# Kernel optimization log

Hardware: AMD Instinct MI355X
Metric: run time of the kernel (lower is better)

Reference implementation:

```python
import jax, jax.numpy as jnp
import numpy as np
import math

NUM_HEADS = 8
SR_RATIO = 2
LN_EPS = 1e-5


def setup_inputs() -> dict:
    key = jax.random.key(0)
    ks = jax.random.split(key, 8)
    B, H, W, C = 2, 64, 64, 512
    N = H * W
    M = (H // SR_RATIO) * (W // SR_RATIO)  # 1024, K/V feature dim after SR reshape
    units = C  # num_heads * head_dim
    s = 0.02
    return {
        "x": jax.random.normal(ks[0], (B, N, C), jnp.float32),
        "Wq": jax.random.normal(ks[1], (C, units), jnp.float32) * s,
        "bq": jnp.zeros((units,), jnp.float32),
        "Wconv": jax.random.normal(ks[2], (C, C, SR_RATIO, SR_RATIO), jnp.float32) * s,  # OIHW
        "bconv": jnp.zeros((C,), jnp.float32),
        "gamma": jnp.ones((M,), jnp.float32),
        "beta": jnp.zeros((M,), jnp.float32),
        "Wkv": jax.random.normal(ks[3], (M, 2 * units), jnp.float32) * s,
        "bkv": jnp.zeros((2 * units,), jnp.float32),
        "Wproj": jax.random.normal(ks[4], (units, C), jnp.float32) * s,
        "bproj": jnp.zeros((C,), jnp.float32),
        "H": H,
        "W": W,
    }


def reference(x, Wq, bq, Wconv, bconv, gamma, beta, Wkv, bkv, Wproj, bproj, H, W):
    B, N, C = x.shape
    nh = NUM_HEADS
    hd = C // nh
    units = nh * hd
    sr = SR_RATIO

    # Q: [B, nh, N, hd]
    q = (x @ Wq + bq).reshape(B, N, nh, hd).transpose(0, 2, 1, 3)

    # Spatial reduction on K/V: x -> [B, C, H, W] -> conv(stride=sr) -> [B, C, H/sr, W/sr]
    xi = x.transpose(0, 2, 1).reshape(B, C, H, W)
    xc = jax.lax.conv_general_dilated(
        xi, Wconv, window_strides=(sr, sr), padding="VALID",
        dimension_numbers=("NCHW", "OIHW", "NCHW"))
    xc = xc + bconv[None, :, None, None]
    x_ = xc.reshape(B, C, -1)  # [B, C, M]; K/V seq len = C, feature dim = M
    mu = jnp.mean(x_, axis=-1, keepdims=True)
    var = jnp.mean(jnp.square(x_ - mu), axis=-1, keepdims=True)
    x_ = (x_ - mu) * jax.lax.rsqrt(var + LN_EPS) * gamma + beta

    # KV: [B, C, 2*units] -> [2, B, nh, C, hd]
    kv = (x_ @ Wkv + bkv).reshape(B, C, 2, nh, hd).transpose(2, 0, 3, 1, 4)
    k, v = kv[0], kv[1]  # each [B, nh, C, hd]

    attn = jnp.einsum("bhnd,bhmd->bhnm", q, k) / jnp.asarray(math.sqrt(hd), x.dtype)
    attn = jax.nn.softmax(attn, axis=-1)  # [B, nh, N, C]

    out = jnp.einsum("bhnm,bhmd->bhnd", attn, v)  # [B, nh, N, hd]
    # Faithful to original: transpose to [B, nh, hd, N] then row-major reshape to [B, N, units]
    out = out.transpose(0, 1, 3, 2).reshape(B, -1, units)
    out = out @ Wproj + bproj  # [B, N, C]
    return out
```

## Files before the change

### kernel.cpp

```cpp
#include <hip/hip_runtime.h>


#define B_    2
#define NTOK  4096
#define C_    512
#define MSP   1024
#define NH    8
#define HD    64

typedef __attribute__((ext_vector_type(8))) short short8;
typedef __attribute__((ext_vector_type(4))) short short4v;
typedef __attribute__((ext_vector_type(4))) float f32x4;

__device__ __forceinline__ unsigned short f2bf(float f) {
    unsigned u = __builtin_bit_cast(unsigned, f);
    u += 0x7FFFu + ((u >> 16) & 1u);
    return (unsigned short)(u >> 16);
}

__global__ __launch_bounds__(256) void convert_bf16(
    const float* __restrict__ in, unsigned short* __restrict__ out, int n8)
{
    int i = blockIdx.x * 256 + threadIdx.x;
    if (i >= n8) return;
    float4 a = ((const float4*)in)[2 * i];
    float4 b = ((const float4*)in)[2 * i + 1];
    short8 o;
    o[0] = (short)f2bf(a.x); o[1] = (short)f2bf(a.y);
    o[2] = (short)f2bf(a.z); o[3] = (short)f2bf(a.w);
    o[4] = (short)f2bf(b.x); o[5] = (short)f2bf(b.y);
    o[6] = (short)f2bf(b.z); o[7] = (short)f2bf(b.w);
    ((short8*)out)[i] = o;
}

__global__ __launch_bounds__(256) void transpose_convert(
    const float* __restrict__ in, unsigned short* __restrict__ out, int R, int C)
{
    __shared__ float T[64][68];
    const int tid = threadIdx.x;
    const int r0 = blockIdx.y * 64, c0 = blockIdx.x * 64;
    const int i = tid >> 2, jp = tid & 3;
    #pragma unroll
    for (int q = 0; q < 4; ++q) {
        float4 v = *(const float4*)(in + (long)(r0 + i) * C + c0 + jp * 16 + q * 4);
        *(float4*)&T[i][jp * 16 + q * 4] = v;
    }
    __syncthreads();
    #pragma unroll
    for (int q = 0; q < 4; ++q) {
        short4v o;
        #pragma unroll
        for (int l = 0; l < 4; ++l)
            o[l] = (short)f2bf(T[jp * 16 + q * 4 + l][i]);
        *(short4v*)(out + (long)(c0 + i) * R + r0 + jp * 16 + q * 4) = o;
    }
}

__global__ __launch_bounds__(256) void gather_kernel(
    const float* __restrict__ x, unsigned short* __restrict__ xg)
{
    const int tid = threadIdx.x;
    const int ty = tid >> 4, tx = tid & 15;
    const int m = blockIdx.x * 16 + ty;
    const int b = blockIdx.y;
    const int my = m >> 5, mx = m & 31;
    const float* xb_ = x + (long)b * NTOK * C_;
    unsigned short* op = xg + ((long)b * MSP + m) * 2048;
    const float* p00 = xb_ + (long)((2 * my + 0) * 64 + 2 * mx + 0) * C_;
    const float* p01 = xb_ + (long)((2 * my + 0) * 64 + 2 * mx + 1) * C_;
    const float* p10 = xb_ + (long)((2 * my + 1) * 64 + 2 * mx + 0) * C_;
    const float* p11 = xb_ + (long)((2 * my + 1) * 64 + 2 * mx + 1) * C_;
    for (int c0 = tx * 4; c0 < C_; c0 += 64) {
        float4 v0 = *(const float4*)(p00 + c0);
        float4 v1 = *(const float4*)(p01 + c0);
        float4 v2 = *(const float4*)(p10 + c0);
        float4 v3 = *(const float4*)(p11 + c0);
        short8 o0, o1;
        o0[0] = (short)f2bf(v0.x); o0[1] = (short)f2bf(v1.x);
        o0[2] = (short)f2bf(v2.x); o0[3] = (short)f2bf(v3.x);
        o0[4] = (short)f2bf(v0.y); o0[5] = (short)f2bf(v1.y);
        o0[6] = (short)f2bf(v2.y); o0[7] = (short)f2bf(v3.y);
        o1[0] = (short)f2bf(v0.z); o1[1] = (short)f2bf(v1.z);
        o1[2] = (short)f2bf(v2.z); o1[3] = (short)f2bf(v3.z);
        o1[4] = (short)f2bf(v0.w); o1[5] = (short)f2bf(v1.w);
        o1[6] = (short)f2bf(v2.w); o1[7] = (short)f2bf(v3.w);
        *(short8*)(op + 4 * c0) = o0;
        *(short8*)(op + 4 * c0 + 8) = o1;
    }
}

template<int OMODE>
__global__ __launch_bounds__(256) void gemm_bf16(
    const unsigned short* __restrict__ A, const unsigned short* __restrict__ BT,
    const float* __restrict__ bias, void* __restrict__ Cv,
    int M, int N, int Kc, int KS, int lda, int ldb, int ldc,
    long sAb, long sBb, long sCb)
{
    __shared__ unsigned short As[128][72];
    __shared__ unsigned short Bs[128][72];
    const int tid = threadIdx.x;
    const int z = blockIdx.z, b = z / KS, kc = z % KS;
    const int row0 = blockIdx.y * 128, col0 = blockIdx.x * 128;
    const unsigned short* Ap = A + b * sAb + (long)kc * Kc + (long)row0 * lda;
    const unsigned short* Bp = BT + b * sBb + (long)kc * Kc + (long)col0 * ldb;
    const int lane = tid & 63, wave = tid >> 6;
    const int wr = (wave >> 1) * 64, wc = (wave & 1) * 64;
    const int l15 = lane & 15, l4 = lane >> 4;

    f32x4 acc[4][4] = {};
    const int nk = Kc >> 6;
    for (int ks = 0; ks < nk; ++ks) {
        const int k0 = ks << 6;
        short8 ar[4], br[4];
        int rr[4], pp[4];
        #pragma unroll
        for (int i = 0; i < 4; ++i) {
            int chunk = tid + 256 * i;
            rr[i] = chunk >> 3; pp[i] = chunk & 7;
            ar[i] = *(const short8*)(Ap + (long)rr[i] * lda + k0 + pp[i] * 8);
            br[i] = *(const short8*)(Bp + (long)rr[i] * ldb + k0 + pp[i] * 8);
        }
        __syncthreads();
        #pragma unroll
        for (int i = 0; i < 4; ++i) {
            *(short8*)&As[rr[i]][pp[i] * 8] = ar[i];
            *(short8*)&Bs[rr[i]][pp[i] * 8] = br[i];
        }
        __syncthreads();
        #pragma unroll
        for (int kg = 0; kg < 2; ++kg) {
            short8 af[4], bf[4];
            #pragma unroll
            for (int mf = 0; mf < 4; ++mf)
                af[mf] = *(const short8*)&As[wr + mf * 16 + l15][kg * 32 + l4 * 8];
            #pragma unroll
            for (int nf = 0; nf < 4; ++nf)
                bf[nf] = *(const short8*)&Bs[wc + nf * 16 + l15][kg * 32 + l4 * 8];
            #pragma unroll
            for (int mf = 0; mf < 4; ++mf)
                #pragma unroll
                for (int nf = 0; nf < 4; ++nf)
                    acc[mf][nf] = __builtin_amdgcn_mfma_f32_16x16x32_bf16(
                        af[mf], bf[nf], acc[mf][nf], 0, 0, 0);
        }
    }
    const int cb = col0 + wc + l15;
    const int rb = row0 + wr + l4 * 4;
    if (OMODE == 0) {
        float* C = (float*)Cv + sCb * b;
        #pragma unroll
        for (int mf = 0; mf < 4; ++mf)
            #pragma unroll
            for (int nf = 0; nf < 4; ++nf)
                #pragma unroll
                for (int i = 0; i < 4; ++i)
                    atomicAdd(&C[(long)(rb + mf * 16 + i) * ldc + cb + nf * 16],
                              acc[mf][nf][i]);
    } else if (OMODE == 1) {
        unsigned short* C = (unsigned short*)Cv + sCb * b;
        #pragma unroll
        for (int nf = 0; nf < 4; ++nf) {
            float bv = bias[cb + nf * 16];
            #pragma unroll
            for (int mf = 0; mf < 4; ++mf)
                #pragma unroll
                for (int i = 0; i < 4; ++i)
                    C[(long)(rb + mf * 16 + i) * ldc + cb + nf * 16] =
                        f2bf(acc[mf][nf][i] + bv);
        }
    } else {
        float* C = (float*)Cv + sCb * b;
        #pragma unroll
        for (int nf = 0; nf < 4; ++nf) {
            float bv = bias[cb + nf * 16];
            #pragma unroll
            for (int mf = 0; mf < 4; ++mf)
                #pragma unroll
                for (int i = 0; i < 4; ++i)
                    C[(long)(rb + mf * 16 + i) * ldc + cb + nf * 16] =
                        acc[mf][nf][i] + bv;
        }
    }
}

__global__ __launch_bounds__(256) void ln_kernel(
    const float* __restrict__ xw, unsigned short* __restrict__ xwb,
    const float* __restrict__ gamma, const float* __restrict__ beta)
{
    __shared__ float red[256];
    const int tid = threadIdx.x;
    const float* p = xw + (long)blockIdx.x * MSP;
    float4 v = ((const float4*)p)[tid];
    red[tid] = v.x + v.y + v.z + v.w;
    __syncthreads();
    for (int off = 128; off > 0; off >>= 1) {
        if (tid < off) red[tid] += red[tid + off];
        __syncthreads();
    }
    float mu = red[0] * (1.0f / MSP);
    __syncthreads();
    float dx = v.x - mu, dy = v.y - mu, dz = v.z - mu, dw = v.w - mu;
    red[tid] = dx * dx + dy * dy + dz * dz + dw * dw;
    __syncthreads();
    for (int off = 128; off > 0; off >>= 1) {
        if (tid < off) red[tid] += red[tid + off];
        __syncthreads();
    }
    float rs = rsqrtf(red[0] * (1.0f / MSP) + 1e-5f);
    int m = tid * 4;
    float4 g  = *(const float4*)(gamma + m);
    float4 be = *(const float4*)(beta + m);
    short4v o;
    o[0] = (short)f2bf(dx * rs * g.x + be.x);
    o[1] = (short)f2bf(dy * rs * g.y + be.y);
    o[2] = (short)f2bf(dz * rs * g.z + be.z);
    o[3] = (short)f2bf(dw * rs * g.w + be.w);
    *(short4v*)(xwb + (long)blockIdx.x * MSP + m) = o;
}

__global__ __launch_bounds__(256) void kvpost_kernel(
    const float* __restrict__ kvtmp, const float* __restrict__ bkv,
    unsigned short* __restrict__ kbuf, unsigned short* __restrict__ vT)
{
    __shared__ float T[64][68];
    const int tid = threadIdx.x;
    const int m0 = blockIdx.x * 64, u0 = blockIdx.y * 64, b = blockIdx.z;
    const float* base = kvtmp + (long)b * 512 * 1024;
    const int i = tid >> 2, jp = tid & 3;
    #pragma unroll
    for (int q = 0; q < 4; ++q) {
        int uc = u0 + jp * 16 + q * 4;
        float4 v  = *(const float4*)(base + (long)(m0 + i) * 1024 + uc);
        float4 bb = *(const float4*)(bkv + uc);
        short4v o;
        o[0] = (short)f2bf(v.x + bb.x); o[1] = (short)f2bf(v.y + bb.y);
        o[2] = (short)f2bf(v.z + bb.z); o[3] = (short)f2bf(v.w + bb.w);
        *(short4v*)(kbuf + ((long)b * 512 + m0 + i) * 512 + uc) = o;
    }
    #pragma unroll
    for (int q = 0; q < 4; ++q) {
        int uc = u0 + jp * 16 + q * 4;
        float4 v  = *(const float4*)(base + (long)(m0 + i) * 1024 + 512 + uc);
        float4 bb = *(const float4*)(bkv + 512 + uc);
        float4 t; t.x = v.x + bb.x; t.y = v.y + bb.y; t.z = v.z + bb.z; t.w = v.w + bb.w;
        *(float4*)&T[i][jp * 16 + q * 4] = t;
    }
    __syncthreads();
    #pragma unroll
    for (int q = 0; q < 4; ++q) {
        short4v o;
        #pragma unroll
        for (int l = 0; l < 4; ++l)
            o[l] = (short)f2bf(T[jp * 16 + q * 4 + l][i]);
        *(short4v*)(vT + ((long)b * 512 + u0 + i) * 512 + m0 + jp * 16 + q * 4) = o;
    }
}

__global__ __launch_bounds__(256) void attn_kernel(
    const unsigned short* __restrict__ qb, const unsigned short* __restrict__ kbuf,
    const unsigned short* __restrict__ vT, unsigned short* __restrict__ o2)
{
    __shared__ unsigned short Qs[128][72];
    __shared__ unsigned short Ks[64][72];
    __shared__ unsigned short Vs[64][72];
    __shared__ unsigned short Ps[4][32][72];
    const int tid = threadIdx.x;
    const int b = blockIdx.y >> 3, h = blockIdx.y & 7;
    const int n0 = blockIdx.x * 128;
    const int lane = tid & 63, w = tid >> 6;
    const int l15 = lane & 15, l4 = lane >> 4;

    const unsigned short* Qg = qb + ((long)b * NTOK + n0) * 512 + h * 64;
    const unsigned short* Kg = kbuf + (long)b * 512 * 512 + h * 64;
    const unsigned short* Vg = vT + ((long)b * 512 + h * 64) * 512;

    #pragma unroll
    for (int it = 0; it < 4; ++it) {
        int chunk = tid + 256 * it;
        int r = chunk >> 3, p = chunk & 7;
        *(short8*)&Qs[r][p * 8] = *(const short8*)(Qg + (long)r * 512 + p * 8);
    }
    __syncthreads();
    short8 qa[2][2];
    #pragma unroll
    for (int mf = 0; mf < 2; ++mf)
        #pragma unroll
        for (int kg = 0; kg < 2; ++kg)
            qa[mf][kg] = *(const short8*)&Qs[w * 32 + mf * 16 + l15][kg * 32 + l4 * 8];

    f32x4 oacc[2][4] = {};
    float lsum[2][4] = {};

    for (int mt = 0; mt < 8; ++mt) {
        const int m0 = mt * 64;
        __syncthreads();
        #pragma unroll
        for (int it = 0; it < 2; ++it) {
            int chunk = tid + 256 * it;
            int r = chunk >> 3, p = chunk & 7;
            *(short8*)&Ks[r][p * 8] = *(const short8*)(Kg + (long)(m0 + r) * 512 + p * 8);
            *(short8*)&Vs[r][p * 8] = *(const short8*)(Vg + (long)r * 512 + m0 + p * 8);
        }
        __syncthreads();
        f32x4 s[2][4];
        #pragma unroll
        for (int nf = 0; nf < 4; ++nf) {
            short8 kb0 = *(const short8*)&Ks[nf * 16 + l15][l4 * 8];
            short8 kb1 = *(const short8*)&Ks[nf * 16 + l15][32 + l4 * 8];
            #pragma unroll
            for (int mf = 0; mf < 2; ++mf) {
                f32x4 zz = {};
                zz = __builtin_amdgcn_mfma_f32_16x16x32_bf16(qa[mf][0], kb0, zz, 0, 0, 0);
                zz = __builtin_amdgcn_mfma_f32_16x16x32_bf16(qa[mf][1], kb1, zz, 0, 0, 0);
                s[mf][nf] = zz;
            }
        }
        #pragma unroll
        for (int mf = 0; mf < 2; ++mf)
            #pragma unroll
            for (int nf = 0; nf < 4; ++nf)
                #pragma unroll
                for (int i = 0; i < 4; ++i) {
                    float pv = __expf(s[mf][nf][i] * 0.125f);
                    lsum[mf][i] += pv;
                    Ps[w][mf * 16 + l4 * 4 + i][nf * 16 + l15] = f2bf(pv);
                }
        #pragma unroll
        for (int mf = 0; mf < 2; ++mf) {
            short8 pa0 = *(const short8*)&Ps[w][mf * 16 + l15][l4 * 8];
            short8 pa1 = *(const short8*)&Ps[w][mf * 16 + l15][32 + l4 * 8];
            #pragma unroll
            for (int df = 0; df < 4; ++df) {
                short8 vb0 = *(const short8*)&Vs[df * 16 + l15][l4 * 8];
                short8 vb1 = *(const short8*)&Vs[df * 16 + l15][32 + l4 * 8];
                oacc[mf][df] = __builtin_amdgcn_mfma_f32_16x16x32_bf16(pa0, vb0, oacc[mf][df], 0, 0, 0);
                oacc[mf][df] = __builtin_amdgcn_mfma_f32_16x16x32_bf16(pa1, vb1, oacc[mf][df], 0, 0, 0);
            }
        }
    }
    #pragma unroll
    for (int mf = 0; mf < 2; ++mf)
        #pragma unroll
        for (int i = 0; i < 4; ++i) {
            float v = lsum[mf][i];
            v += __shfl_xor(v, 1, 64);
            v += __shfl_xor(v, 2, 64);
            v += __shfl_xor(v, 4, 64);
            v += __shfl_xor(v, 8, 64);
            lsum[mf][i] = 1.0f / v;
        }
    const int nhi = n0 >> 9;
    const int colb = (n0 & 511) + w * 32;
    #pragma unroll
    for (int mf = 0; mf < 2; ++mf)
        #pragma unroll
        for (int df = 0; df < 4; ++df) {
            int d = h * 64 + df * 16 + l15;
            long row = (long)b * NTOK + (long)d * 8 + nhi;
            short4v o;
            o[0] = (short)f2bf(oacc[mf][df][0] * lsum[mf][0]);
            o[1] = (short)f2bf(oacc[mf][df][1] * lsum[mf][1]);
            o[2] = (short)f2bf(oacc[mf][df][2] * lsum[mf][2]);
            o[3] = (short)f2bf(oacc[mf][df][3] * lsum[mf][3]);
            *(short4v*)(o2 + row * 512 + colb + mf * 16 + l4 * 4) = o;
        }
}

extern "C" void kernel_launch(void* const* d_in, const int* in_sizes, int n_in,
                              void* d_out, int out_size, void* d_ws, size_t ws_size,
                              hipStream_t stream)
{
    (void)in_sizes; (void)n_in; (void)out_size; (void)ws_size;
    const float* x     = (const float*)d_in[0];
    const float* Wq    = (const float*)d_in[1];
    const float* bq    = (const float*)d_in[2];
    const float* Wconv = (const float*)d_in[3];
    const float* gamma = (const float*)d_in[5];
    const float* beta  = (const float*)d_in[6];
    const float* Wkv   = (const float*)d_in[7];
    const float* bkv   = (const float*)d_in[8];
    const float* Wproj = (const float*)d_in[9];
    const float* bproj = (const float*)d_in[10];
    float* out = (float*)d_out;
    char* ws = (char*)d_ws;

    unsigned short* xb     = (unsigned short*)(ws);
    unsigned short* qbuf   = (unsigned short*)(ws + (8u << 20));
    unsigned short* xg     = (unsigned short*)(ws + (16u << 20));
    unsigned short* o2     = xg;
    unsigned short* WqT    = (unsigned short*)(ws + (24u << 20));
    unsigned short* WcB    = (unsigned short*)(ws + (24u << 20) + (512u << 10));
    unsigned short* WkvT   = (unsigned short*)(ws + (27u << 20) - (512u << 10));
    unsigned short* WprojT = (unsigned short*)(ws + (29u << 20) - (512u << 10));
    float*          xw     = (float*)         (ws + (29u << 20));
    unsigned short* xwb    = (unsigned short*)(ws + (33u << 20));
    float*          kvtmp  = (float*)         (ws + (35u << 20));
    unsigned short* kbuf   = (unsigned short*)(ws + (39u << 20));
    unsigned short* vTb    = (unsigned short*)(ws + (40u << 20));

    hipMemsetAsync(xw,    0, 2l * 512 * 1024 * 4, stream);
    hipMemsetAsync(kvtmp, 0, 2l * 512 * 1024 * 4, stream);

    convert_bf16<<<dim3(2048), 256, 0, stream>>>(x, xb, 4194304 / 8);
    convert_bf16<<<dim3(512),  256, 0, stream>>>(Wconv, WcB, 1048576 / 8);
    transpose_convert<<<dim3(8, 8),   256, 0, stream>>>(Wq,    WqT,    512, 512);
    transpose_convert<<<dim3(16, 16), 256, 0, stream>>>(Wkv,   WkvT,   1024, 1024);
    transpose_convert<<<dim3(8, 8),   256, 0, stream>>>(Wproj, WprojT, 512, 512);
    gather_kernel<<<dim3(64, 2), 256, 0, stream>>>(x, xg);

    gemm_bf16<1><<<dim3(4, 64, 1), 256, 0, stream>>>(
        xb, WqT, bq, qbuf, 8192, 512, 512, 1, 512, 512, 512, 0, 0, 0);
    gemm_bf16<0><<<dim3(8, 4, 8), 256, 0, stream>>>(
        WcB, xg, nullptr, xw, 512, 1024, 512, 4, 2048, 2048, 1024,
        0, 2048l * 1024, 512l * 1024);
    ln_kernel<<<dim3(1024), 256, 0, stream>>>(xw, xwb, gamma, beta);
    gemm_bf16<0><<<dim3(8, 4, 8), 256, 0, stream>>>(
        xwb, WkvT, nullptr, kvtmp, 512, 1024, 256, 4, 1024, 1024, 1024,
        512l * 1024, 0, 512l * 1024);
    kvpost_kernel<<<dim3(8, 8, 2), 256, 0, stream>>>(kvtmp, bkv, kbuf, vTb);
    attn_kernel<<<dim3(32, 16), 256, 0, stream>>>(qbuf, kbuf, vTb, o2);
    gemm_bf16<2><<<dim3(4, 64, 1), 256, 0, stream>>>(
        o2, WprojT, bproj, out, 8192, 512, 512, 1, 512, 512, 512, 0, 0, 0);
}
```

Before: 210.0 us.

## Replace split-K atomics with partial buffers and fuse x conversion into gather

The split-K GEMMs now write each K-chunk's partial result to its own slice with plain stores instead of atomicAdd. The following LayerNorm and kv-post kernels sum the four partials as they read them. This removes two memsets and the atomic traffic, at the cost of more workspace and more reads in the consumers. The separate conversion of x to bf16 is folded into the gather kernel, which already reads every x element once, so one full pass over x is dropped.

After: 192.4 us. 8.3% less time.

```diff
diff --git a/kernel.cpp b/kernel.cpp
--- a/kernel.cpp
+++ b/kernel.cpp
@@ -57,7 +57,8 @@
 }
 
 __global__ __launch_bounds__(256) void gather_kernel(
-    const float* __restrict__ x, unsigned short* __restrict__ xg)
+    const float* __restrict__ x, unsigned short* __restrict__ xg,
+    unsigned short* __restrict__ xb)
 {
     const int tid = threadIdx.x;
     const int ty = tid >> 4, tx = tid & 15;
@@ -66,10 +67,13 @@
     const int my = m >> 5, mx = m & 31;
     const float* xb_ = x + (long)b * NTOK * C_;
     unsigned short* op = xg + ((long)b * MSP + m) * 2048;
-    const float* p00 = xb_ + (long)((2 * my + 0) * 64 + 2 * mx + 0) * C_;
-    const float* p01 = xb_ + (long)((2 * my + 0) * 64 + 2 * mx + 1) * C_;
-    const float* p10 = xb_ + (long)((2 * my + 1) * 64 + 2 * mx + 0) * C_;
-    const float* p11 = xb_ + (long)((2 * my + 1) * 64 + 2 * mx + 1) * C_;
+    unsigned short* xo = xb + (long)b * NTOK * C_;
+    const int n00 = (2 * my) * 64 + 2 * mx;
+    const int n01 = n00 + 1, n10 = n00 + 64, n11 = n00 + 65;
+    const float* p00 = xb_ + (long)n00 * C_;
+    const float* p01 = xb_ + (long)n01 * C_;
+    const float* p10 = xb_ + (long)n10 * C_;
+    const float* p11 = xb_ + (long)n11 * C_;
     for (int c0 = tx * 4; c0 < C_; c0 += 64) {
         float4 v0 = *(const float4*)(p00 + c0);
         float4 v1 = *(const float4*)(p01 + c0);
@@ -86,6 +90,19 @@
         o1[6] = (short)f2bf(v2.w); o1[7] = (short)f2bf(v3.w);
         *(short8*)(op + 4 * c0) = o0;
         *(short8*)(op + 4 * c0 + 8) = o1;
+        short4v s;
+        s[0] = (short)f2bf(v0.x); s[1] = (short)f2bf(v0.y);
+        s[2] = (short)f2bf(v0.z); s[3] = (short)f2bf(v0.w);
+        *(short4v*)(xo + (long)n00 * C_ + c0) = s;
+        s[0] = (short)f2bf(v1.x); s[1] = (short)f2bf(v1.y);
+        s[2] = (short)f2bf(v1.z); s[3] = (short)f2bf(v1.w);
+        *(short4v*)(xo + (long)n01 * C_ + c0) = s;
+        s[0] = (short)f2bf(v2.x); s[1] = (short)f2bf(v2.y);
+        s[2] = (short)f2bf(v2.z); s[3] = (short)f2bf(v2.w);
+        *(short4v*)(xo + (long)n10 * C_ + c0) = s;
+        s[0] = (short)f2bf(v3.x); s[1] = (short)f2bf(v3.y);
+        s[2] = (short)f2bf(v3.z); s[3] = (short)f2bf(v3.w);
+        *(short4v*)(xo + (long)n11 * C_ + c0) = s;
     }
 }
 
@@ -147,15 +164,14 @@
     const int cb = col0 + wc + l15;
     const int rb = row0 + wr + l4 * 4;
     if (OMODE == 0) {
-        float* C = (float*)Cv + sCb * b;
+        float* C = (float*)Cv + (long)z * M * (long)ldc;
         #pragma unroll
         for (int mf = 0; mf < 4; ++mf)
             #pragma unroll
             for (int nf = 0; nf < 4; ++nf)
                 #pragma unroll
                 for (int i = 0; i < 4; ++i)
-                    atomicAdd(&C[(long)(rb + mf * 16 + i) * ldc + cb + nf * 16],
-                              acc[mf][nf][i]);
+                    C[(long)(rb + mf * 16 + i) * ldc + cb + nf * 16] = acc[mf][nf][i];
     } else if (OMODE == 1) {
         unsigned short* C = (unsigned short*)Cv + sCb * b;
         #pragma unroll
@@ -184,13 +200,20 @@
 }
 
 __global__ __launch_bounds__(256) void ln_kernel(
-    const float* __restrict__ xw, unsigned short* __restrict__ xwb,
+    const float* __restrict__ pconv, unsigned short* __restrict__ xwb,
     const float* __restrict__ gamma, const float* __restrict__ beta)
 {
     __shared__ float red[256];
     const int tid = threadIdx.x;
-    const float* p = xw + (long)blockIdx.x * MSP;
-    float4 v = ((const float4*)p)[tid];
+    const int b = blockIdx.x >> 9, c = blockIdx.x & 511;
+    const float* base = pconv + ((long)b * 4 * 512 + c) * 1024;
+    const int m = tid * 4;
+    float4 v = make_float4(0.f, 0.f, 0.f, 0.f);
+    #pragma unroll
+    for (int kc = 0; kc < 4; ++kc) {
+        float4 t = *(const float4*)(base + (long)kc * 512 * 1024 + m);
+        v.x += t.x; v.y += t.y; v.z += t.z; v.w += t.w;
+    }
     red[tid] = v.x + v.y + v.z + v.w;
     __syncthreads();
     for (int off = 128; off > 0; off >>= 1) {
@@ -207,7 +230,6 @@
         __syncthreads();
     }
     float rs = rsqrtf(red[0] * (1.0f / MSP) + 1e-5f);
-    int m = tid * 4;
     float4 g  = *(const float4*)(gamma + m);
     float4 be = *(const float4*)(beta + m);
     short4v o;
@@ -219,31 +241,40 @@
 }
 
 __global__ __launch_bounds__(256) void kvpost_kernel(
-    const float* __restrict__ kvtmp, const float* __restrict__ bkv,
+    const float* __restrict__ pkv, const float* __restrict__ bkv,
     unsigned short* __restrict__ kbuf, unsigned short* __restrict__ vT)
 {
     __shared__ float T[64][68];
     const int tid = threadIdx.x;
     const int m0 = blockIdx.x * 64, u0 = blockIdx.y * 64, b = blockIdx.z;
-    const float* base = kvtmp + (long)b * 512 * 1024;
+    const float* base = pkv + (long)b * 4 * 512 * 1024;
     const int i = tid >> 2, jp = tid & 3;
     #pragma unroll
     for (int q = 0; q < 4; ++q) {
         int uc = u0 + jp * 16 + q * 4;
-        float4 v  = *(const float4*)(base + (long)(m0 + i) * 1024 + uc);
         float4 bb = *(const float4*)(bkv + uc);
+        float4 v = bb;
+        #pragma unroll
+        for (int kc = 0; kc < 4; ++kc) {
+            float4 t = *(const float4*)(base + (long)kc * 512 * 1024 + (long)(m0 + i) * 1024 + uc);
+            v.x += t.x; v.y += t.y; v.z += t.z; v.w += t.w;
+        }
         short4v o;
-        o[0] = (short)f2bf(v.x + bb.x); o[1] = (short)f2bf(v.y + bb.y);
-        o[2] = (short)f2bf(v.z + bb.z); o[3] = (short)f2bf(v.w + bb.w);
+        o[0] = (short)f2bf(v.x); o[1] = (short)f2bf(v.y);
+        o[2] = (short)f2bf(v.z); o[3] = (short)f2bf(v.w);
         *(short4v*)(kbuf + ((long)b * 512 + m0 + i) * 512 + uc) = o;
     }
     #pragma unroll
     for (int q = 0; q < 4; ++q) {
         int uc = u0 + jp * 16 + q * 4;
-        float4 v  = *(const float4*)(base + (long)(m0 + i) * 1024 + 512 + uc);
         float4 bb = *(const float4*)(bkv + 512 + uc);
-        float4 t; t.x = v.x + bb.x; t.y = v.y + bb.y; t.z = v.z + bb.z; t.w = v.w + bb.w;
-        *(float4*)&T[i][jp * 16 + q * 4] = t;
+        float4 v = bb;
+        #pragma unroll
+        for (int kc = 0; kc < 4; ++kc) {
+            float4 t = *(const float4*)(base + (long)kc * 512 * 1024 + (long)(m0 + i) * 1024 + 512 + uc);
+            v.x += t.x; v.y += t.y; v.z += t.z; v.w += t.w;
+        }
+        *(float4*)&T[i][jp * 16 + q * 4] = v;
     }
     __syncthreads();
     #pragma unroll
@@ -385,39 +416,35 @@
     char* ws = (char*)d_ws;
 
     unsigned short* xb     = (unsigned short*)(ws);
-    unsigned short* qbuf   = (unsigned short*)(ws + (8u << 20));
-    unsigned short* xg     = (unsigned short*)(ws + (16u << 20));
+    unsigned short* qbuf   = (unsigned short*)(ws + (8ul  << 20));
+    unsigned short* xg     = (unsigned short*)(ws + (16ul << 20));
     unsigned short* o2     = xg;
-    unsigned short* WqT    = (unsigned short*)(ws + (24u << 20));
-    unsigned short* WcB    = (unsigned short*)(ws + (24u << 20) + (512u << 10));
-    unsigned short* WkvT   = (unsigned short*)(ws + (27u << 20) - (512u << 10));
-    unsigned short* WprojT = (unsigned short*)(ws + (29u << 20) - (512u << 10));
-    float*          xw     = (float*)         (ws + (29u << 20));
-    unsigned short* xwb    = (unsigned short*)(ws + (33u << 20));
-    float*          kvtmp  = (float*)         (ws + (35u << 20));
-    unsigned short* kbuf   = (unsigned short*)(ws + (39u << 20));
-    unsigned short* vTb    = (unsigned short*)(ws + (40u << 20));
-
-    hipMemsetAsync(xw,    0, 2l * 512 * 1024 * 4, stream);
-    hipMemsetAsync(kvtmp, 0, 2l * 512 * 1024 * 4, stream);
-
-    convert_bf16<<<dim3(2048), 256, 0, stream>>>(x, xb, 4194304 / 8);
+    unsigned short* WqT    = (unsigned short*)(ws + (24ul << 20));
+    unsigned short* WcB    = (unsigned short*)(ws + (25ul << 20));
+    unsigned short* WkvT   = (unsigned short*)(ws + (27ul << 20));
+    unsigned short* WprojT = (unsigned short*)(ws + (29ul << 20));
+    float*          pconv  = (float*)         (ws + (30ul << 20));
+    unsigned short* xwb    = (unsigned short*)(ws + (46ul << 20));
+    float*          pkv    = (float*)         (ws + (48ul << 20));
+    unsigned short* kbuf   = (unsigned short*)(ws + (64ul << 20));
+    unsigned short* vTb    = (unsigned short*)(ws + (65ul << 20));
+
     convert_bf16<<<dim3(512),  256, 0, stream>>>(Wconv, WcB, 1048576 / 8);
     transpose_convert<<<dim3(8, 8),   256, 0, stream>>>(Wq,    WqT,    512, 512);
     transpose_convert<<<dim3(16, 16), 256, 0, stream>>>(Wkv,   WkvT,   1024, 1024);
     transpose_convert<<<dim3(8, 8),   256, 0, stream>>>(Wproj, WprojT, 512, 512);
-    gather_kernel<<<dim3(64, 2), 256, 0, stream>>>(x, xg);
+    gather_kernel<<<dim3(64, 2), 256, 0, stream>>>(x, xg, xb);
 
     gemm_bf16<1><<<dim3(4, 64, 1), 256, 0, stream>>>(
         xb, WqT, bq, qbuf, 8192, 512, 512, 1, 512, 512, 512, 0, 0, 0);
     gemm_bf16<0><<<dim3(8, 4, 8), 256, 0, stream>>>(
-        WcB, xg, nullptr, xw, 512, 1024, 512, 4, 2048, 2048, 1024,
-        0, 2048l * 1024, 512l * 1024);
-    ln_kernel<<<dim3(1024), 256, 0, stream>>>(xw, xwb, gamma, beta);
+        WcB, xg, nullptr, pconv, 512, 1024, 512, 4, 2048, 2048, 1024,
+        0, 2048l * 1024, 0);
+    ln_kernel<<<dim3(1024), 256, 0, stream>>>(pconv, xwb, gamma, beta);
     gemm_bf16<0><<<dim3(8, 4, 8), 256, 0, stream>>>(
-        xwb, WkvT, nullptr, kvtmp, 512, 1024, 256, 4, 1024, 1024, 1024,
-        512l * 1024, 0, 512l * 1024);
-    kvpost_kernel<<<dim3(8, 8, 2), 256, 0, stream>>>(kvtmp, bkv, kbuf, vTb);
+        xwb, WkvT, nullptr, pkv, 512, 1024, 256, 4, 1024, 1024, 1024,
+        512l * 1024, 0, 0);
+    kvpost_kernel<<<dim3(8, 8, 2), 256, 0, stream>>>(pkv, bkv, kbuf, vTb);
     attn_kernel<<<dim3(32, 16), 256, 0, stream>>>(qbuf, kbuf, vTb, o2);
     gemm_bf16<2><<<dim3(4, 64, 1), 256, 0, stream>>>(
         o2, WprojT, bproj, out, 8192, 512, 512, 1, 512, 512, 512, 0, 0, 0);
```
